# Kernel tuning notes

Hardware: AMD Instinct MI355X
Metric: run time of the kernel (lower is better)

## Reference

```python
import jax, jax.numpy as jnp
import numpy as np

B, S, D, F = 8, 2048, 256, 8

def setup_inputs() -> dict:
    key = jax.random.key(0)
    ks = jax.random.split(key, 7)
    hidden_states = jax.random.normal(ks[0], (B, S, D), dtype=jnp.float32)
    # flat indices into zero-prepended [1 + B*S, D] token table; 0 = padding row
    select_idx = jax.random.randint(ks[1], (B, S, F), 0, B * S + 1, dtype=jnp.int32)
    word_mask = jax.random.randint(ks[2], (B, S), 0, 2, dtype=jnp.int32)
    W1 = jax.random.normal(ks[3], (D, D), dtype=jnp.float32) * (1.0 / np.sqrt(D))
    b1 = jax.random.normal(ks[4], (D,), dtype=jnp.float32) * 0.02
    w2 = jax.random.normal(ks[5], (D,), dtype=jnp.float32) * (1.0 / np.sqrt(D))
    b2 = jax.random.normal(ks[6], (1,), dtype=jnp.float32) * 0.02
    return {"hidden_states": hidden_states, "select_idx": select_idx,
            "word_mask": word_mask, "W1": W1, "b1": b1, "w2": w2, "b2": b2}

def reference(hidden_states, select_idx, word_mask, W1, b1, w2, b2):
    b, s, d = hidden_states.shape
    h = jnp.tanh(hidden_states.reshape(-1, d) @ W1.T + b1)          # [B*S, D]
    h = jnp.concatenate([jnp.zeros((1, d), h.dtype), h], axis=0)    # zero padding row at index 0
    g = h[select_idx.reshape(-1)]                                    # gather: [B*S*F, D]
    g = g.reshape(b * s, -1, d).max(axis=1)                          # AdaptiveMaxPool1d(1) over word occurrences
    scores = (g @ w2 + b2[0]).reshape(b, s)                          # w2 linear -> [B, S]
    neg = -10000.0 * (1.0 - word_mask.astype(jnp.float32))
    return scores.astype(jnp.float32) + neg
```

## Files before the change

kernel.cpp:

```cpp
#include <hip/hip_runtime.h>
#include <hip/hip_bf16.h>
#include <math.h>

#define BB 8
#define SS 2048
#define DD 256
#define FF 8
#define NTOK (BB*SS)

typedef __bf16 bf16x8 __attribute__((ext_vector_type(8)));
typedef float  f32x4  __attribute__((ext_vector_type(4)));
typedef float  f32x2  __attribute__((ext_vector_type(2)));

__device__ __forceinline__ unsigned pack2_bf16(float a, float b) {
    return (__float_as_uint(a) >> 16) | (__float_as_uint(b) & 0xFFFF0000u);
}

__global__ __launch_bounds__(256) void w1_to_bf16_kernel(
    const float* __restrict__ W1, unsigned short* __restrict__ W1b)
{
    int i = blockIdx.x * 256 + threadIdx.x;
    f32x4 a = *(const f32x4*)&W1[(size_t)i * 8];
    f32x4 b = *(const f32x4*)&W1[(size_t)i * 8 + 4];
    uint4 p;
    p.x = pack2_bf16(a.x, a.y); p.y = pack2_bf16(a.z, a.w);
    p.z = pack2_bf16(b.x, b.y); p.w = pack2_bf16(b.z, b.w);
    *(uint4*)&W1b[(size_t)i * 8] = p;
}

#define BM 32

__device__ __forceinline__ float fast_tanh(float x) {
    float e = __expf(2.0f * x);
    return 1.0f - 2.0f * __builtin_amdgcn_rcpf(e + 1.0f);
}

__device__ __forceinline__ unsigned char f32_to_fp8(float v) {
    return (unsigned char)(__builtin_amdgcn_cvt_pk_fp8_f32(v, v, 0, false) & 0xFF);
}

__global__ __launch_bounds__(512, 4) void gemm_tanh_kernel(
    const float* __restrict__ x, const unsigned short* __restrict__ W1b,
    const float* __restrict__ b1, unsigned char* __restrict__ table)
{
    __shared__ __align__(16) unsigned short xs[BM * DD];

    const int tid  = threadIdx.x;
    const int bx   = blockIdx.x;
    const int tok0 = bx * BM;

    if (bx == 0 && tid < 64) ((unsigned int*)table)[tid] = 0u;

    const int wave = tid >> 6, lane = tid & 63;
    const int n0 = wave * 32;
    const int lr = lane & 15;
    const int kg = lane >> 4;

    #pragma unroll
    for (int p = 0; p < 4; ++p) {
        int s = p * 512 + tid;
        int row = s >> 6, k4 = s & 63;
        f32x4 v = *(const f32x4*)&x[(size_t)(tok0 + row) * DD + k4 * 4];
        uint2 pk;
        pk.x = pack2_bf16(v.x, v.y);
        pk.y = pack2_bf16(v.z, v.w);
        int g  = k4 >> 1;
        int gp = g ^ (row & 7);
        *(uint2*)&xs[row * DD + gp * 8 + (k4 & 1) * 4] = pk;
    }
    __syncthreads();

    f32x4 acc[2][2];
    #pragma unroll
    for (int mf = 0; mf < 2; ++mf)
        #pragma unroll
        for (int nf = 0; nf < 2; ++nf)
            acc[mf][nf] = (f32x4){0.f, 0.f, 0.f, 0.f};

    const unsigned short* wrow0 = W1b + (size_t)(n0 + lr) * DD + kg * 8;
    const unsigned short* wrow1 = W1b + (size_t)(n0 + 16 + lr) * DD + kg * 8;
    const int sw = lr & 7;

    #pragma unroll
    for (int c = 0; c < 8; ++c) {
        int g   = c * 4 + kg;
        int gp8 = (g ^ sw) * 8;
        bf16x8 af0 = *(const bf16x8*)&xs[lr * DD + gp8];
        bf16x8 af1 = *(const bf16x8*)&xs[(16 + lr) * DD + gp8];
        bf16x8 bf0 = *(const bf16x8*)&wrow0[c * 32];
        bf16x8 bf1 = *(const bf16x8*)&wrow1[c * 32];
        acc[0][0] = __builtin_amdgcn_mfma_f32_16x16x32_bf16(af0, bf0, acc[0][0], 0, 0, 0);
        acc[0][1] = __builtin_amdgcn_mfma_f32_16x16x32_bf16(af0, bf1, acc[0][1], 0, 0, 0);
        acc[1][0] = __builtin_amdgcn_mfma_f32_16x16x32_bf16(af1, bf0, acc[1][0], 0, 0, 0);
        acc[1][1] = __builtin_amdgcn_mfma_f32_16x16x32_bf16(af1, bf1, acc[1][1], 0, 0, 0);
    }

    float bj0 = b1[n0 + lr];
    float bj1 = b1[n0 + 16 + lr];

    __syncthreads();
    unsigned char* sc = (unsigned char*)&xs[0];
    #pragma unroll
    for (int mf = 0; mf < 2; ++mf) {
        #pragma unroll
        for (int nf = 0; nf < 2; ++nf) {
            #pragma unroll
            for (int r = 0; r < 4; ++r) {
                int row = mf * 16 + kg * 4 + r;
                int col = n0 + nf * 16 + lr;
                float v = fast_tanh(acc[mf][nf][r] + (nf ? bj1 : bj0));
                sc[row * 272 + col] = f32_to_fp8(v);
            }
        }
    }
    __syncthreads();
    {
        int row = tid >> 4;
        int off = (tid & 15) * 16;
        uint4 v = *(const uint4*)&sc[row * 272 + off];
        *(uint4*)&table[(size_t)(1 + tok0 + row) * DD + off] = v;
    }
}

__global__ __launch_bounds__(256) void gather_score_kernel(
    const unsigned char* __restrict__ table,
    const int* __restrict__ select_idx,
    const int* __restrict__ word_mask,
    const float* __restrict__ w2,
    const float* __restrict__ b2,
    float* __restrict__ out)
{
    const int tid  = threadIdx.x;
    const int lane = tid & 63;
    const int wv   = tid >> 6;
    const int i    = blockIdx.x * 4 + wv;
    const int half = lane >> 5;
    const int c    = lane & 31;
    const int d0   = c * 8;

    const int4* sp = (const int4*)(select_idx + (size_t)i * FF);
    int4 q0 = sp[0], q1 = sp[1];
    int rows[4];
    rows[0] = half ? q0.y : q0.x;
    rows[1] = half ? q0.w : q0.z;
    rows[2] = half ? q1.y : q1.x;
    rows[3] = half ? q1.w : q1.z;

    float m[8];
    #pragma unroll
    for (int j = 0; j < 8; ++j) m[j] = -INFINITY;

    #pragma unroll
    for (int it = 0; it < 4; ++it) {
        uint2 u = *(const uint2*)(table + (size_t)rows[it] * DD + d0);
        f32x2 a0 = __builtin_amdgcn_cvt_pk_f32_fp8(u.x, false);
        f32x2 a1 = __builtin_amdgcn_cvt_pk_f32_fp8(u.x, true);
        f32x2 a2 = __builtin_amdgcn_cvt_pk_f32_fp8(u.y, false);
        f32x2 a3 = __builtin_amdgcn_cvt_pk_f32_fp8(u.y, true);
        m[0] = fmaxf(m[0], a0.x); m[1] = fmaxf(m[1], a0.y);
        m[2] = fmaxf(m[2], a1.x); m[3] = fmaxf(m[3], a1.y);
        m[4] = fmaxf(m[4], a2.x); m[5] = fmaxf(m[5], a2.y);
        m[6] = fmaxf(m[6], a3.x); m[7] = fmaxf(m[7], a3.y);
    }

    #pragma unroll
    for (int j = 0; j < 8; ++j) m[j] = fmaxf(m[j], __shfl_xor(m[j], 32));

    f32x4 wa = *(const f32x4*)&w2[d0];
    f32x4 wb = *(const f32x4*)&w2[d0 + 4];
    float p = m[0] * wa.x + m[1] * wa.y + m[2] * wa.z + m[3] * wa.w
            + m[4] * wb.x + m[5] * wb.y + m[6] * wb.z + m[7] * wb.w;

    #pragma unroll
    for (int off = 16; off; off >>= 1) p += __shfl_xor(p, off);

    if (lane == 0) {
        float neg = word_mask[i] ? 0.f : -10000.f;
        out[i] = p + b2[0] + neg;
    }
}

extern "C" void kernel_launch(void* const* d_in, const int* in_sizes, int n_in,
                              void* d_out, int out_size, void* d_ws, size_t ws_size,
                              hipStream_t stream) {
    const float* hs    = (const float*)d_in[0];
    const int*   sidx  = (const int*)  d_in[1];
    const int*   wmask = (const int*)  d_in[2];
    const float* W1    = (const float*)d_in[3];
    const float* b1    = (const float*)d_in[4];
    const float* w2    = (const float*)d_in[5];
    const float* b2    = (const float*)d_in[6];
    float* out = (float*)d_out;

    unsigned char*  table = (unsigned char*)d_ws;
    unsigned short* W1b   = (unsigned short*)((char*)d_ws + (8u << 20));

    w1_to_bf16_kernel<<<32, 256, 0, stream>>>(W1, W1b);
    gemm_tanh_kernel<<<NTOK / BM, 512, 0, stream>>>(hs, W1b, b1, table);
    gather_score_kernel<<<NTOK / 4, 256, 0, stream>>>(table, sidx, wmask, w2, b2, out);
}
```

Baseline: 90.46 us.

## Fuse three kernels into one persistent cooperative kernel with grid syncs

Replaces the W1 conversion, GEMM+tanh and gather/score kernels with a single cooperative persistent kernel. Each phase loops over its work with a grid-stride, and the phases are separated by grid.sync. The aim is to remove two kernel launch gaps and tail effects. In exchange it adds grid-wide barrier cost, and the grid size is limited by occupancy, which may lower parallelism in the gather phase.

```diff
diff --git a/kernel.cpp b/kernel.cpp
--- a/kernel.cpp
+++ b/kernel.cpp
@@ -1,6 +1,9 @@
 #include <hip/hip_runtime.h>
+#include <hip/hip_cooperative_groups.h>
 #include <hip/hip_bf16.h>
 #include <math.h>
+
+namespace cg = cooperative_groups;
 
 #define BB 8
 #define SS 2048
@@ -8,6 +11,9 @@
 #define FF 8
 #define NTOK (BB*SS)
 
+#define BM 32
+#define NGRP (NTOK/BM)
+
 typedef __bf16 bf16x8 __attribute__((ext_vector_type(8)));
 typedef float  f32x4  __attribute__((ext_vector_type(4)));
 typedef float  f32x2  __attribute__((ext_vector_type(2)));
@@ -15,168 +21,167 @@
 __device__ __forceinline__ unsigned pack2_bf16(float a, float b) {
     return (__float_as_uint(a) >> 16) | (__float_as_uint(b) & 0xFFFF0000u);
 }
-
-__global__ __launch_bounds__(256) void w1_to_bf16_kernel(
-    const float* __restrict__ W1, unsigned short* __restrict__ W1b)
-{
-    int i = blockIdx.x * 256 + threadIdx.x;
-    f32x4 a = *(const f32x4*)&W1[(size_t)i * 8];
-    f32x4 b = *(const f32x4*)&W1[(size_t)i * 8 + 4];
-    uint4 p;
-    p.x = pack2_bf16(a.x, a.y); p.y = pack2_bf16(a.z, a.w);
-    p.z = pack2_bf16(b.x, b.y); p.w = pack2_bf16(b.z, b.w);
-    *(uint4*)&W1b[(size_t)i * 8] = p;
-}
-
-#define BM 32
-
 __device__ __forceinline__ float fast_tanh(float x) {
     float e = __expf(2.0f * x);
     return 1.0f - 2.0f * __builtin_amdgcn_rcpf(e + 1.0f);
 }
-
 __device__ __forceinline__ unsigned char f32_to_fp8(float v) {
     return (unsigned char)(__builtin_amdgcn_cvt_pk_fp8_f32(v, v, 0, false) & 0xFF);
 }
 
-__global__ __launch_bounds__(512, 4) void gemm_tanh_kernel(
-    const float* __restrict__ x, const unsigned short* __restrict__ W1b,
-    const float* __restrict__ b1, unsigned char* __restrict__ table)
+__global__ __launch_bounds__(512, 4) void mega_kernel(
+    const float* __restrict__ x, const float* __restrict__ W1,
+    const float* __restrict__ b1,
+    const int* __restrict__ select_idx, const int* __restrict__ word_mask,
+    const float* __restrict__ w2, const float* __restrict__ b2,
+    unsigned char* __restrict__ table, unsigned short* __restrict__ W1b,
+    float* __restrict__ out)
 {
     __shared__ __align__(16) unsigned short xs[BM * DD];
 
-    const int tid  = threadIdx.x;
-    const int bx   = blockIdx.x;
-    const int tok0 = bx * BM;
-
-    if (bx == 0 && tid < 64) ((unsigned int*)table)[tid] = 0u;
+    cg::grid_group grid = cg::this_grid();
+    const int tid = threadIdx.x;
+    const int bx  = blockIdx.x;
+    const int nb  = gridDim.x;
+
+    {
+        int gt = bx * 512 + tid;
+        for (int i = gt; i < (DD * DD / 8); i += nb * 512) {
+            f32x4 a = *(const f32x4*)&W1[(size_t)i * 8];
+            f32x4 b = *(const f32x4*)&W1[(size_t)i * 8 + 4];
+            uint4 p;
+            p.x = pack2_bf16(a.x, a.y); p.y = pack2_bf16(a.z, a.w);
+            p.z = pack2_bf16(b.x, b.y); p.w = pack2_bf16(b.z, b.w);
+            *(uint4*)&W1b[(size_t)i * 8] = p;
+        }
+        if (gt < 64) ((unsigned int*)table)[gt] = 0u;
+    }
+    __threadfence();
+    grid.sync();
 
     const int wave = tid >> 6, lane = tid & 63;
     const int n0 = wave * 32;
     const int lr = lane & 15;
     const int kg = lane >> 4;
-
-    #pragma unroll
-    for (int p = 0; p < 4; ++p) {
-        int s = p * 512 + tid;
-        int row = s >> 6, k4 = s & 63;
-        f32x4 v = *(const f32x4*)&x[(size_t)(tok0 + row) * DD + k4 * 4];
-        uint2 pk;
-        pk.x = pack2_bf16(v.x, v.y);
-        pk.y = pack2_bf16(v.z, v.w);
-        int g  = k4 >> 1;
-        int gp = g ^ (row & 7);
-        *(uint2*)&xs[row * DD + gp * 8 + (k4 & 1) * 4] = pk;
+    const int sw = lr & 7;
+
+    for (int g = bx; g < NGRP; g += nb) {
+        const int tok0 = g * BM;
+        __syncthreads();
+
+        #pragma unroll
+        for (int p = 0; p < 4; ++p) {
+            int s = p * 512 + tid;
+            int row = s >> 6, k4 = s & 63;
+            f32x4 v = *(const f32x4*)&x[(size_t)(tok0 + row) * DD + k4 * 4];
+            uint2 pk;
+            pk.x = pack2_bf16(v.x, v.y);
+            pk.y = pack2_bf16(v.z, v.w);
+            int gq = k4 >> 1;
+            int gp = gq ^ (row & 7);
+            *(uint2*)&xs[row * DD + gp * 8 + (k4 & 1) * 4] = pk;
+        }
+        __syncthreads();
+
+        f32x4 acc[2][2];
+        #pragma unroll
+        for (int mf = 0; mf < 2; ++mf)
+            #pragma unroll
+            for (int nf = 0; nf < 2; ++nf)
+                acc[mf][nf] = (f32x4){0.f, 0.f, 0.f, 0.f};
+
+        const unsigned short* wrow0 = W1b + (size_t)(n0 + lr) * DD + kg * 8;
+        const unsigned short* wrow1 = W1b + (size_t)(n0 + 16 + lr) * DD + kg * 8;
+
+        #pragma unroll
+        for (int c = 0; c < 8; ++c) {
+            int gp8 = ((c * 4 + kg) ^ sw) * 8;
+            bf16x8 af0 = *(const bf16x8*)&xs[lr * DD + gp8];
+            bf16x8 af1 = *(const bf16x8*)&xs[(16 + lr) * DD + gp8];
+            bf16x8 bf0 = *(const bf16x8*)&wrow0[c * 32];
+            bf16x8 bf1 = *(const bf16x8*)&wrow1[c * 32];
+            acc[0][0] = __builtin_amdgcn_mfma_f32_16x16x32_bf16(af0, bf0, acc[0][0], 0, 0, 0);
+            acc[0][1] = __builtin_amdgcn_mfma_f32_16x16x32_bf16(af0, bf1, acc[0][1], 0, 0, 0);
+            acc[1][0] = __builtin_amdgcn_mfma_f32_16x16x32_bf16(af1, bf0, acc[1][0], 0, 0, 0);
+            acc[1][1] = __builtin_amdgcn_mfma_f32_16x16x32_bf16(af1, bf1, acc[1][1], 0, 0, 0);
+        }
+
+        float bj0 = b1[n0 + lr];
+        float bj1 = b1[n0 + 16 + lr];
+
+        __syncthreads();
+        unsigned char* sc = (unsigned char*)&xs[0];
+        #pragma unroll
+        for (int mf = 0; mf < 2; ++mf) {
+            #pragma unroll
+            for (int nf = 0; nf < 2; ++nf) {
+                #pragma unroll
+                for (int r = 0; r < 4; ++r) {
+                    int row = mf * 16 + kg * 4 + r;
+                    int col = n0 + nf * 16 + lr;
+                    float v = fast_tanh(acc[mf][nf][r] + (nf ? bj1 : bj0));
+                    sc[row * 272 + col] = f32_to_fp8(v);
+                }
+            }
+        }
+        __syncthreads();
+        {
+            int row = tid >> 4;
+            int off = (tid & 15) * 16;
+            uint4 v = *(const uint4*)&sc[row * 272 + off];
+            *(uint4*)&table[(size_t)(1 + tok0 + row) * DD + off] = v;
+        }
     }
-    __syncthreads();
-
-    f32x4 acc[2][2];
-    #pragma unroll
-    for (int mf = 0; mf < 2; ++mf)
-        #pragma unroll
-        for (int nf = 0; nf < 2; ++nf)
-            acc[mf][nf] = (f32x4){0.f, 0.f, 0.f, 0.f};
-
-    const unsigned short* wrow0 = W1b + (size_t)(n0 + lr) * DD + kg * 8;
-    const unsigned short* wrow1 = W1b + (size_t)(n0 + 16 + lr) * DD + kg * 8;
-    const int sw = lr & 7;
-
-    #pragma unroll
-    for (int c = 0; c < 8; ++c) {
-        int g   = c * 4 + kg;
-        int gp8 = (g ^ sw) * 8;
-        bf16x8 af0 = *(const bf16x8*)&xs[lr * DD + gp8];
-        bf16x8 af1 = *(const bf16x8*)&xs[(16 + lr) * DD + gp8];
-        bf16x8 bf0 = *(const bf16x8*)&wrow0[c * 32];
-        bf16x8 bf1 = *(const bf16x8*)&wrow1[c * 32];
-        acc[0][0] = __builtin_amdgcn_mfma_f32_16x16x32_bf16(af0, bf0, acc[0][0], 0, 0, 0);
-        acc[0][1] = __builtin_amdgcn_mfma_f32_16x16x32_bf16(af0, bf1, acc[0][1], 0, 0, 0);
-        acc[1][0] = __builtin_amdgcn_mfma_f32_16x16x32_bf16(af1, bf0, acc[1][0], 0, 0, 0);
-        acc[1][1] = __builtin_amdgcn_mfma_f32_16x16x32_bf16(af1, bf1, acc[1][1], 0, 0, 0);
-    }
-
-    float bj0 = b1[n0 + lr];
-    float bj1 = b1[n0 + 16 + lr];
-
-    __syncthreads();
-    unsigned char* sc = (unsigned char*)&xs[0];
-    #pragma unroll
-    for (int mf = 0; mf < 2; ++mf) {
-        #pragma unroll
-        for (int nf = 0; nf < 2; ++nf) {
-            #pragma unroll
-            for (int r = 0; r < 4; ++r) {
-                int row = mf * 16 + kg * 4 + r;
-                int col = n0 + nf * 16 + lr;
-                float v = fast_tanh(acc[mf][nf][r] + (nf ? bj1 : bj0));
-                sc[row * 272 + col] = f32_to_fp8(v);
-            }
-        }
-    }
-    __syncthreads();
-    {
-        int row = tid >> 4;
-        int off = (tid & 15) * 16;
-        uint4 v = *(const uint4*)&sc[row * 272 + off];
-        *(uint4*)&table[(size_t)(1 + tok0 + row) * DD + off] = v;
-    }
-}
-
-__global__ __launch_bounds__(256) void gather_score_kernel(
-    const unsigned char* __restrict__ table,
-    const int* __restrict__ select_idx,
-    const int* __restrict__ word_mask,
-    const float* __restrict__ w2,
-    const float* __restrict__ b2,
-    float* __restrict__ out)
-{
-    const int tid  = threadIdx.x;
-    const int lane = tid & 63;
-    const int wv   = tid >> 6;
-    const int i    = blockIdx.x * 4 + wv;
+    __threadfence();
+    grid.sync();
+
     const int half = lane >> 5;
-    const int c    = lane & 31;
-    const int d0   = c * 8;
-
-    const int4* sp = (const int4*)(select_idx + (size_t)i * FF);
-    int4 q0 = sp[0], q1 = sp[1];
-    int rows[4];
-    rows[0] = half ? q0.y : q0.x;
-    rows[1] = half ? q0.w : q0.z;
-    rows[2] = half ? q1.y : q1.x;
-    rows[3] = half ? q1.w : q1.z;
-
-    float m[8];
-    #pragma unroll
-    for (int j = 0; j < 8; ++j) m[j] = -INFINITY;
-
-    #pragma unroll
-    for (int it = 0; it < 4; ++it) {
-        uint2 u = *(const uint2*)(table + (size_t)rows[it] * DD + d0);
-        f32x2 a0 = __builtin_amdgcn_cvt_pk_f32_fp8(u.x, false);
-        f32x2 a1 = __builtin_amdgcn_cvt_pk_f32_fp8(u.x, true);
-        f32x2 a2 = __builtin_amdgcn_cvt_pk_f32_fp8(u.y, false);
-        f32x2 a3 = __builtin_amdgcn_cvt_pk_f32_fp8(u.y, true);
-        m[0] = fmaxf(m[0], a0.x); m[1] = fmaxf(m[1], a0.y);
-        m[2] = fmaxf(m[2], a1.x); m[3] = fmaxf(m[3], a1.y);
-        m[4] = fmaxf(m[4], a2.x); m[5] = fmaxf(m[5], a2.y);
-        m[6] = fmaxf(m[6], a3.x); m[7] = fmaxf(m[7], a3.y);
-    }
-
-    #pragma unroll
-    for (int j = 0; j < 8; ++j) m[j] = fmaxf(m[j], __shfl_xor(m[j], 32));
-
-    f32x4 wa = *(const f32x4*)&w2[d0];
-    f32x4 wb = *(const f32x4*)&w2[d0 + 4];
-    float p = m[0] * wa.x + m[1] * wa.y + m[2] * wa.z + m[3] * wa.w
-            + m[4] * wb.x + m[5] * wb.y + m[6] * wb.z + m[7] * wb.w;
-
-    #pragma unroll
-    for (int off = 16; off; off >>= 1) p += __shfl_xor(p, off);
-
-    if (lane == 0) {
-        float neg = word_mask[i] ? 0.f : -10000.f;
-        out[i] = p + b2[0] + neg;
+    const int cc   = lane & 31;
+    const int d0   = cc * 8;
+
+    for (int t0 = bx * 8; t0 < NTOK; t0 += nb * 8) {
+        const int i = t0 + wave;
+
+        const int4* sp = (const int4*)(select_idx + (size_t)i * FF);
+        int4 q0 = sp[0], q1 = sp[1];
+        int rows[4];
+        rows[0] = half ? q0.y : q0.x;
+        rows[1] = half ? q0.w : q0.z;
+        rows[2] = half ? q1.y : q1.x;
+        rows[3] = half ? q1.w : q1.z;
+
+        float m[8];
+        #pragma unroll
+        for (int j = 0; j < 8; ++j) m[j] = -INFINITY;
+
+        #pragma unroll
+        for (int it = 0; it < 4; ++it) {
+            uint2 u = *(const uint2*)(table + (size_t)rows[it] * DD + d0);
+            f32x2 a0 = __builtin_amdgcn_cvt_pk_f32_fp8(u.x, false);
+            f32x2 a1 = __builtin_amdgcn_cvt_pk_f32_fp8(u.x, true);
+            f32x2 a2 = __builtin_amdgcn_cvt_pk_f32_fp8(u.y, false);
+            f32x2 a3 = __builtin_amdgcn_cvt_pk_f32_fp8(u.y, true);
+            m[0] = fmaxf(m[0], a0.x); m[1] = fmaxf(m[1], a0.y);
+            m[2] = fmaxf(m[2], a1.x); m[3] = fmaxf(m[3], a1.y);
+            m[4] = fmaxf(m[4], a2.x); m[5] = fmaxf(m[5], a2.y);
+            m[6] = fmaxf(m[6], a3.x); m[7] = fmaxf(m[7], a3.y);
+        }
+
+        #pragma unroll
+        for (int j = 0; j < 8; ++j) m[j] = fmaxf(m[j], __shfl_xor(m[j], 32));
+
+        f32x4 wa = *(const f32x4*)&w2[d0];
+        f32x4 wb = *(const f32x4*)&w2[d0 + 4];
+        float p = m[0] * wa.x + m[1] * wa.y + m[2] * wa.z + m[3] * wa.w
+                + m[4] * wb.x + m[5] * wb.y + m[6] * wb.z + m[7] * wb.w;
+
+        #pragma unroll
+        for (int off = 16; off; off >>= 1) p += __shfl_xor(p, off);
+
+        if (lane == 0) {
+            float neg = word_mask[i] ? 0.f : -10000.f;
+            out[i] = p + b2[0] + neg;
+        }
     }
 }
 
@@ -195,7 +200,14 @@
     unsigned char*  table = (unsigned char*)d_ws;
     unsigned short* W1b   = (unsigned short*)((char*)d_ws + (8u << 20));
 
-    w1_to_bf16_kernel<<<32, 256, 0, stream>>>(W1, W1b);
-    gemm_tanh_kernel<<<NTOK / BM, 512, 0, stream>>>(hs, W1b, b1, table);
-    gather_score_kernel<<<NTOK / 4, 256, 0, stream>>>(table, sidx, wmask, w2, b2, out);
-}
+    int nbpc = 0;
+    if (hipOccupancyMaxActiveBlocksPerMultiprocessor(&nbpc, mega_kernel, 512, 0)
+            != hipSuccess || nbpc < 1)
+        nbpc = 1;
+    int grid = nbpc * 256;
+    if (grid > NGRP) grid = NGRP;
+
+    void* args[] = {(void*)&hs, (void*)&W1, (void*)&b1, (void*)&sidx, (void*)&wmask,
+                    (void*)&w2, (void*)&b2, (void*)&table, (void*)&W1b, (void*)&out};
+    hipLaunchCooperativeKernel(mega_kernel, dim3(grid), dim3(512), args, 0, stream);
+}
```

New measurement: 231.9 us. 2.56x slower.
